# Optimization experiments

Hardware: AMD Instinct MI355X
Metric: run time of the kernel (lower is better)

The kernel has to match this reference:

```python
import jax, jax.numpy as jnp
import numpy as np


def setup_inputs() -> dict:
    key = jax.random.key(0)
    k_x, k_c = jax.random.split(key)
    ROWS, COLS = 4, 4
    B, N = 1024, 224
    x = jax.random.normal(k_x, (B, N, N), dtype=jnp.float32)
    # kaiming_normal_ on [rows, cols]: std = sqrt(2 / fan_in) with fan_in = cols
    coef = jax.random.normal(k_c, (ROWS, COLS), dtype=jnp.float32) * np.sqrt(2.0 / COLS)
    return {"x": x, "coef": coef}


def reference(x, coef):
    # x: [B, N, N]; coef: [rows, cols]
    rows, cols = coef.shape
    B, N, _ = x.shape

    # a_series[i] = matrix_power(x, i+2) for i in 0..rows-1 (the original also
    # computes power rows+2 but never uses it). Only the diagonals are needed:
    # diag(A ** p) == diag(A) ** p for elementwise power p.
    def step(P, _):
        Pn = jnp.matmul(P, x)                      # next matrix power, [B, N, N]
        return Pn, jnp.diagonal(Pn, axis1=-2, axis2=-1)  # [B, N]

    _, diags = jax.lax.scan(step, x, None, length=rows)  # [rows, B, N]
    d = jnp.transpose(diags, (1, 0, 2))                  # [B, rows, N]

    # traces[b, i, j] = sum_n diag(x^{i+2})[b, n] ** (j+1)
    exps = jnp.arange(1, cols + 1)                       # [cols]
    traces = jnp.sum(d[..., None] ** exps, axis=2)       # [B, rows, cols]

    # norm[i, j] = (N*N) ** (i + j + 2), computed in float (the original's int64
    # pow overflows for any realistic N; float is the intended math)
    i = jnp.arange(rows, dtype=x.dtype)[:, None]
    j = jnp.arange(cols, dtype=x.dtype)[None, :]
    norm = jnp.asarray(float(N * N), x.dtype) ** (i + j + 2.0)  # [rows, cols]

    return jnp.sum(coef * traces / norm, axis=(-1, -2))  # [B]
```

## Files before the change

kernel.cpp:

```cpp
#include <hip/hip_runtime.h>
#include <stdint.h>

#define B_ 1024
#define N_ 224
#define NN_ (N_ * N_)

typedef unsigned short u16;
typedef unsigned int u32;
typedef __attribute__((ext_vector_type(8))) short s8v;
typedef __attribute__((ext_vector_type(4))) float f4v;

__device__ __forceinline__ u16 f2bf(float f) {
  u32 u = __float_as_uint(f);
  u = (u + 0x7FFFu + ((u >> 16) & 1u)) >> 16;
  return (u16)u;
}
__device__ __forceinline__ float bf2f(u16 h) { return __uint_as_float((u32)h << 16); }
__device__ __forceinline__ float rec(u16 h, u16 l) { return bf2f(h) + bf2f(l); }

__device__ __forceinline__ void gload16(const void* g, void* l) {
  __builtin_amdgcn_global_load_lds(
      (const __attribute__((address_space(1))) uint32_t*)g,
      (__attribute__((address_space(3))) uint32_t*)l, 16, 0, 0);
}

__global__ __launch_bounds__(256) void splitT(const float* __restrict__ x,
                                              u16* __restrict__ xh, u16* __restrict__ xl,
                                              u16* __restrict__ xhT, u16* __restrict__ xlT) {
  __shared__ u16 th[32][34];
  __shared__ u16 tl[32][34];
  const int bid = blockIdx.x;
  const int mat = bid / 49, t2 = bid % 49;
  const int tm = (t2 / 7) * 32, tn = (t2 % 7) * 32;
  const int t = threadIdx.x;
  const int r = t >> 3, c4 = (t & 7) << 2;
  const size_t o = (size_t)mat * NN_ + (size_t)(tm + r) * N_ + tn + c4;
  const float4 v = *(const float4*)(x + o);
  u16 h0 = f2bf(v.x), h1 = f2bf(v.y), h2 = f2bf(v.z), h3 = f2bf(v.w);
  u16 l0 = f2bf(v.x - bf2f(h0)), l1 = f2bf(v.y - bf2f(h1));
  u16 l2 = f2bf(v.z - bf2f(h2)), l3 = f2bf(v.w - bf2f(h3));
  ushort4 hv = {h0, h1, h2, h3}, lv = {l0, l1, l2, l3};
  *(ushort4*)(xh + o) = hv;
  *(ushort4*)(xl + o) = lv;
  th[r][c4] = h0; th[r][c4 + 1] = h1; th[r][c4 + 2] = h2; th[r][c4 + 3] = h3;
  tl[r][c4] = l0; tl[r][c4 + 1] = l1; tl[r][c4 + 2] = l2; tl[r][c4 + 3] = l3;
  __syncthreads();
  ushort4 thv = {th[c4][r], th[c4 + 1][r], th[c4 + 2][r], th[c4 + 3][r]};
  ushort4 tlv = {tl[c4][r], tl[c4 + 1][r], tl[c4 + 2][r], tl[c4 + 3][r]};
  const size_t oT = (size_t)mat * NN_ + (size_t)(tn + r) * N_ + tm + c4;
  *(ushort4*)(xhT + oT) = thv;
  *(ushort4*)(xlT + oT) = tlv;
}

__global__ __launch_bounds__(256, 2) void gemmNT(const u16* __restrict__ Ah, const u16* __restrict__ Al,
                                                 const u16* __restrict__ BTh, const u16* __restrict__ BTl,
                                                 u16* __restrict__ Ch, u16* __restrict__ Cl) {
  __shared__ __align__(16) u16 As[2][128][64];
  __shared__ __align__(16) u16 Bs[2][128][64];

  const int nwg = gridDim.x, bid = blockIdx.x;
  const int q = nwg >> 3, rr = nwg & 7, xcd = bid & 7, pos = bid >> 3;
  const int wg = (xcd < rr) ? (xcd * (q + 1) + pos) : (rr * (q + 1) + (xcd - rr) * q + pos);
  const int mat = wg >> 2, t2 = wg & 3;
  const int m0 = (t2 & 1) * 96, n0 = (t2 >> 1) * 96;
  const size_t mo = (size_t)mat * NN_;
  const u16* A0 = Ah + mo;
  const u16* A1 = Al + mo;
  const u16* B0 = BTh + mo;
  const u16* B1 = BTl + mo;

  const int t = threadIdx.x;
  const int l = t & 63, w = t >> 6;
  const int wm = w & 1, wn = w >> 1;
  const int lg = l >> 4, l15 = l & 15;

  f4v acc[4][4];
#pragma unroll
  for (int i = 0; i < 4; ++i)
#pragma unroll
    for (int j = 0; j < 4; ++j) acc[i][j] = (f4v){0.f, 0.f, 0.f, 0.f};

  auto stage = [&](int buf, int k0) {
#pragma unroll
    for (int i = 0; i < 4; ++i) {
      const int s = i * 256 + t;
      const int row = s >> 3, p = s & 7;
      const int c = p ^ (row & 7);
      const int g = c & 3;
      const u16* ga = (c < 4) ? A0 : A1;
      const u16* gb = (c < 4) ? B0 : B1;
      gload16(ga + (size_t)(m0 + row) * N_ + k0 + g * 8, &As[buf][row][p * 8]);
      gload16(gb + (size_t)(n0 + row) * N_ + k0 + g * 8, &Bs[buf][row][p * 8]);
    }
  };

  stage(0, 0);
  int cur = 0;
  for (int kt = 0; kt < 7; ++kt) {
    __syncthreads();
    if (kt < 6) stage(cur ^ 1, (kt + 1) * 32);
    const u16(*Ab)[64] = As[cur];
    const u16(*Bb)[64] = Bs[cur];
    s8v ah[4], al[4], bh[4], bl[4];
#pragma unroll
    for (int i = 0; i < 4; ++i) {
      const int ra = wm * 64 + i * 16 + l15;
      const int rb = wn * 64 + i * 16 + l15;
      ah[i] = *(const s8v*)&Ab[ra][(lg ^ (ra & 7)) * 8];
      al[i] = *(const s8v*)&Ab[ra][((4 + lg) ^ (ra & 7)) * 8];
      bh[i] = *(const s8v*)&Bb[rb][(lg ^ (rb & 7)) * 8];
      bl[i] = *(const s8v*)&Bb[rb][((4 + lg) ^ (rb & 7)) * 8];
    }
#pragma unroll
    for (int i = 0; i < 4; ++i)
#pragma unroll
      for (int j = 0; j < 4; ++j) {
        acc[i][j] = __builtin_amdgcn_mfma_f32_16x16x32_bf16(ah[i], bh[j], acc[i][j], 0, 0, 0);
        acc[i][j] = __builtin_amdgcn_mfma_f32_16x16x32_bf16(ah[i], bl[j], acc[i][j], 0, 0, 0);
        acc[i][j] = __builtin_amdgcn_mfma_f32_16x16x32_bf16(al[i], bh[j], acc[i][j], 0, 0, 0);
      }
    cur ^= 1;
  }

  u16* cph = Ch + mo;
  u16* cpl = Cl + mo;
#pragma unroll
  for (int i = 0; i < 4; ++i)
#pragma unroll
    for (int j = 0; j < 4; ++j)
#pragma unroll
      for (int qd = 0; qd < 4; ++qd) {
        const float v = acc[i][j][qd];
        const int row = m0 + wm * 64 + i * 16 + lg * 4 + qd;
        const int col = n0 + wn * 64 + j * 16 + l15;
        const u16 hh = f2bf(v);
        const u16 ll = f2bf(v - bf2f(hh));
        cph[(size_t)row * N_ + col] = hh;
        cpl[(size_t)row * N_ + col] = ll;
      }
}

__global__ __launch_bounds__(256) void diagk(const u16* __restrict__ P2h, const u16* __restrict__ P2l,
                                             const u16* __restrict__ P3h, const u16* __restrict__ P3l,
                                             float* __restrict__ dg, int bBase) {
  __shared__ float s2[N_][17];
  __shared__ float s3[N_][17];
  const int b = blockIdx.x;
  const size_t mo = (size_t)b * NN_;
  const u16 *p2h = P2h + mo, *p2l = P2l + mo, *p3h = P3h + mo, *p3l = P3l + mo;
  const int gb = bBase + b;
  const int t = threadIdx.x;
  float d4 = 0.f, d5 = 0.f;
  for (int kb = 0; kb < N_; kb += 16) {
    __syncthreads();
#pragma unroll
    for (int base = 0; base < N_ * 16; base += 256) {
      const int f = base + t;
      const int n = f >> 4, j = f & 15;
      const size_t idx = (size_t)n * N_ + kb + j;
      s2[n][j] = rec(p2h[idx], p2l[idx]);
      s3[n][j] = rec(p3h[idx], p3l[idx]);
    }
    __syncthreads();
    if (t < N_) {
#pragma unroll
      for (int j = 0; j < 16; ++j) {
        const size_t ci = (size_t)(kb + j) * N_ + t;
        const float c2 = rec(p2h[ci], p2l[ci]);
        d4 = fmaf(s2[t][j], c2, d4);
        d5 = fmaf(s3[t][j], c2, d5);
      }
    }
  }
  if (t < N_) {
    const size_t di = (size_t)t * N_ + t;
    dg[((size_t)0 * B_ + gb) * N_ + t] = rec(p2h[di], p2l[di]);
    dg[((size_t)1 * B_ + gb) * N_ + t] = rec(p3h[di], p3l[di]);
    dg[((size_t)2 * B_ + gb) * N_ + t] = d4;
    dg[((size_t)3 * B_ + gb) * N_ + t] = d5;
  }
}

__global__ __launch_bounds__(256) void combine(const float* __restrict__ dg,
                                               const float* __restrict__ coef,
                                               float* __restrict__ out) {
  const int lane = threadIdx.x & 63;
  const int b = blockIdx.x * 4 + (threadIdx.x >> 6);
  float T[4][4] = {};
  for (int n = lane; n < N_; n += 64) {
#pragma unroll
    for (int i = 0; i < 4; ++i) {
      const float d = dg[((size_t)i * B_ + b) * N_ + n];
      float p = d;
#pragma unroll
      for (int j = 0; j < 4; ++j) {
        T[i][j] += p;
        p *= d;
      }
    }
  }
#pragma unroll
  for (int i = 0; i < 4; ++i)
#pragma unroll
    for (int j = 0; j < 4; ++j)
#pragma unroll
      for (int s = 32; s > 0; s >>= 1) T[i][j] += __shfl_xor(T[i][j], s, 64);
  if (lane == 0) {
    double acc = 0.0;
#pragma unroll
    for (int i = 0; i < 4; ++i)
#pragma unroll
      for (int j = 0; j < 4; ++j) {
        double norm = 1.0;
        for (int e = 0; e < i + j + 2; ++e) norm *= (double)(N_ * N_);
        acc += (double)coef[i * 4 + j] * ((double)T[i][j] / norm);
      }
    out[b] = (float)acc;
  }
}

extern "C" void kernel_launch(void* const* d_in, const int* in_sizes, int n_in,
                              void* d_out, int out_size, void* d_ws, size_t ws_size,
                              hipStream_t stream) {
  (void)in_sizes; (void)n_in; (void)out_size;
  const float* x = (const float*)d_in[0];
  const float* coef = (const float*)d_in[1];
  float* out = (float*)d_out;
  char* ws = (char*)d_ws;

  size_t off = 0;
  auto alloc = [&](size_t bytes) -> void* {
    off = (off + 255) & ~(size_t)255;
    void* p = ws + off;
    off += bytes;
    return p;
  };

  float* dg = (float*)alloc((size_t)4 * B_ * N_ * sizeof(float));

  const size_t perMat = (size_t)8 * NN_ * sizeof(u16);
  size_t avail = (ws_size > off + 256) ? (ws_size - off - 256) : 0;
  long long Cc = (long long)(avail / perMat);
  if (Cc < 1) Cc = 1;
  if (Cc > B_) Cc = B_;
  const int C = (int)Cc;
  const size_t matEls = (size_t)C * NN_;
  u16* xh = (u16*)alloc(matEls * 2);
  u16* xl = (u16*)alloc(matEls * 2);
  u16* xhT = (u16*)alloc(matEls * 2);
  u16* xlT = (u16*)alloc(matEls * 2);
  u16* P2h = (u16*)alloc(matEls * 2);
  u16* P2l = (u16*)alloc(matEls * 2);
  u16* P3h = (u16*)alloc(matEls * 2);
  u16* P3l = (u16*)alloc(matEls * 2);

  for (int b0 = 0; b0 < B_; b0 += C) {
    const int cb = (B_ - b0 < C) ? (B_ - b0) : C;
    splitT<<<49 * cb, 256, 0, stream>>>(x + (size_t)b0 * NN_, xh, xl, xhT, xlT);
    gemmNT<<<4 * cb, 256, 0, stream>>>(xh, xl, xhT, xlT, P2h, P2l);
    gemmNT<<<4 * cb, 256, 0, stream>>>(P2h, P2l, xhT, xlT, P3h, P3l);
    diagk<<<cb, 256, 0, stream>>>(P2h, P2l, P3h, P3l, dg, b0);
  }
  combine<<<256, 256, 0, stream>>>(dg, coef, out);
}
```

Measured before the change: 1.117 ms.

## Emit transposed P2 from GEMM epilogue and parallelize diagonal reduction across blocks

The first GEMM now also writes a transposed copy of P^2 (hi/lo bf16), so the diagonal kernel can compute row-dot-products of P2·P2 and P3·P2 with contiguous vectorized loads instead of LDS staging and strided column reads. The diag kernel is split into 7 blocks per matrix, with 8 lanes per row and a shuffle reduction, giving much more parallelism than one block per matrix. The cost is extra global writes from the GEMM epilogue (strided ushort4 stores) and a larger workspace per matrix, which may shrink the batch chunk size.

```diff
diff --git a/kernel.cpp b/kernel.cpp
--- a/kernel.cpp
+++ b/kernel.cpp
@@ -9,6 +9,7 @@
 typedef unsigned int u32;
 typedef __attribute__((ext_vector_type(8))) short s8v;
 typedef __attribute__((ext_vector_type(4))) float f4v;
+typedef __attribute__((ext_vector_type(8))) unsigned short us8;
 
 __device__ __forceinline__ u16 f2bf(float f) {
   u32 u = __float_as_uint(f);
@@ -54,7 +55,8 @@
 
 __global__ __launch_bounds__(256, 2) void gemmNT(const u16* __restrict__ Ah, const u16* __restrict__ Al,
                                                  const u16* __restrict__ BTh, const u16* __restrict__ BTl,
-                                                 u16* __restrict__ Ch, u16* __restrict__ Cl) {
+                                                 u16* __restrict__ Ch, u16* __restrict__ Cl,
+                                                 u16* __restrict__ CTh, u16* __restrict__ CTl) {
   __shared__ __align__(16) u16 As[2][128][64];
   __shared__ __align__(16) u16 Bs[2][128][64];
 
@@ -127,57 +129,73 @@
 #pragma unroll
   for (int i = 0; i < 4; ++i)
 #pragma unroll
-    for (int j = 0; j < 4; ++j)
+    for (int j = 0; j < 4; ++j) {
+      u16 hq[4], lq[4];
 #pragma unroll
       for (int qd = 0; qd < 4; ++qd) {
         const float v = acc[i][j][qd];
+        hq[qd] = f2bf(v);
+        lq[qd] = f2bf(v - bf2f(hq[qd]));
         const int row = m0 + wm * 64 + i * 16 + lg * 4 + qd;
         const int col = n0 + wn * 64 + j * 16 + l15;
-        const u16 hh = f2bf(v);
-        const u16 ll = f2bf(v - bf2f(hh));
-        cph[(size_t)row * N_ + col] = hh;
-        cpl[(size_t)row * N_ + col] = ll;
-      }
+        cph[(size_t)row * N_ + col] = hq[qd];
+        cpl[(size_t)row * N_ + col] = lq[qd];
+      }
+      if (CTh) {
+        const int row0 = m0 + wm * 64 + i * 16 + lg * 4;
+        const int col = n0 + wn * 64 + j * 16 + l15;
+        const ushort4 hv = {hq[0], hq[1], hq[2], hq[3]};
+        const ushort4 lv = {lq[0], lq[1], lq[2], lq[3]};
+        *(ushort4*)(CTh + mo + (size_t)col * N_ + row0) = hv;
+        *(ushort4*)(CTl + mo + (size_t)col * N_ + row0) = lv;
+      }
+    }
 }
 
 __global__ __launch_bounds__(256) void diagk(const u16* __restrict__ P2h, const u16* __restrict__ P2l,
+                                             const u16* __restrict__ P2Th, const u16* __restrict__ P2Tl,
                                              const u16* __restrict__ P3h, const u16* __restrict__ P3l,
                                              float* __restrict__ dg, int bBase) {
-  __shared__ float s2[N_][17];
-  __shared__ float s3[N_][17];
-  const int b = blockIdx.x;
+  const int bid = blockIdx.x;
+  const int b = bid / 7, p = bid % 7;
   const size_t mo = (size_t)b * NN_;
-  const u16 *p2h = P2h + mo, *p2l = P2l + mo, *p3h = P3h + mo, *p3l = P3l + mo;
   const int gb = bBase + b;
   const int t = threadIdx.x;
-  float d4 = 0.f, d5 = 0.f;
-  for (int kb = 0; kb < N_; kb += 16) {
-    __syncthreads();
-#pragma unroll
-    for (int base = 0; base < N_ * 16; base += 256) {
-      const int f = base + t;
-      const int n = f >> 4, j = f & 15;
-      const size_t idx = (size_t)n * N_ + kb + j;
-      s2[n][j] = rec(p2h[idx], p2l[idx]);
-      s3[n][j] = rec(p3h[idx], p3l[idx]);
-    }
-    __syncthreads();
-    if (t < N_) {
-#pragma unroll
-      for (int j = 0; j < 16; ++j) {
-        const size_t ci = (size_t)(kb + j) * N_ + t;
-        const float c2 = rec(p2h[ci], p2l[ci]);
-        d4 = fmaf(s2[t][j], c2, d4);
-        d5 = fmaf(s3[t][j], c2, d5);
-      }
-    }
-  }
-  if (t < N_) {
-    const size_t di = (size_t)t * N_ + t;
-    dg[((size_t)0 * B_ + gb) * N_ + t] = rec(p2h[di], p2l[di]);
-    dg[((size_t)1 * B_ + gb) * N_ + t] = rec(p3h[di], p3l[di]);
-    dg[((size_t)2 * B_ + gb) * N_ + t] = d4;
-    dg[((size_t)3 * B_ + gb) * N_ + t] = d5;
+  const int r8 = t >> 3, sub = t & 7;
+  const int n = p * 32 + r8;
+  const int gd = n >> 3;
+
+  float d4 = 0.f, d5 = 0.f, d2 = 0.f, d3 = 0.f;
+  bool own = false;
+  for (int g = sub; g < 28; g += 8) {
+    const size_t gi = mo + (size_t)n * N_ + g * 8;
+    const us8 a2h = *(const us8*)(P2h + gi), a2l = *(const us8*)(P2l + gi);
+    const us8 tth = *(const us8*)(P2Th + gi), ttl = *(const us8*)(P2Tl + gi);
+    const us8 a3h = *(const us8*)(P3h + gi), a3l = *(const us8*)(P3l + gi);
+#pragma unroll
+    for (int i = 0; i < 8; ++i) {
+      const float tv = rec(tth[i], ttl[i]);
+      d4 = fmaf(rec(a2h[i], a2l[i]), tv, d4);
+      d5 = fmaf(rec(a3h[i], a3l[i]), tv, d5);
+    }
+    if (g == gd) {
+      own = true;
+      d2 = rec(a2h[n & 7], a2l[n & 7]);
+      d3 = rec(a3h[n & 7], a3l[n & 7]);
+    }
+  }
+#pragma unroll
+  for (int m = 1; m < 8; m <<= 1) {
+    d4 += __shfl_xor(d4, m, 64);
+    d5 += __shfl_xor(d5, m, 64);
+  }
+  if (sub == 0) {
+    dg[((size_t)2 * B_ + gb) * N_ + n] = d4;
+    dg[((size_t)3 * B_ + gb) * N_ + n] = d5;
+  }
+  if (own) {
+    dg[((size_t)0 * B_ + gb) * N_ + n] = d2;
+    dg[((size_t)1 * B_ + gb) * N_ + n] = d3;
   }
 }
 
@@ -238,7 +256,7 @@
 
   float* dg = (float*)alloc((size_t)4 * B_ * N_ * sizeof(float));
 
-  const size_t perMat = (size_t)8 * NN_ * sizeof(u16);
+  const size_t perMat = (size_t)10 * NN_ * sizeof(u16);
   size_t avail = (ws_size > off + 256) ? (ws_size - off - 256) : 0;
   long long Cc = (long long)(avail / perMat);
   if (Cc < 1) Cc = 1;
@@ -251,15 +269,17 @@
   u16* xlT = (u16*)alloc(matEls * 2);
   u16* P2h = (u16*)alloc(matEls * 2);
   u16* P2l = (u16*)alloc(matEls * 2);
+  u16* P2Th = (u16*)alloc(matEls * 2);
+  u16* P2Tl = (u16*)alloc(matEls * 2);
   u16* P3h = (u16*)alloc(matEls * 2);
   u16* P3l = (u16*)alloc(matEls * 2);
 
   for (int b0 = 0; b0 < B_; b0 += C) {
     const int cb = (B_ - b0 < C) ? (B_ - b0) : C;
     splitT<<<49 * cb, 256, 0, stream>>>(x + (size_t)b0 * NN_, xh, xl, xhT, xlT);
-    gemmNT<<<4 * cb, 256, 0, stream>>>(xh, xl, xhT, xlT, P2h, P2l);
-    gemmNT<<<4 * cb, 256, 0, stream>>>(P2h, P2l, xhT, xlT, P3h, P3l);
-    diagk<<<cb, 256, 0, stream>>>(P2h, P2l, P3h, P3l, dg, b0);
+    gemmNT<<<4 * cb, 256, 0, stream>>>(xh, xl, xhT, xlT, P2h, P2l, P2Th, P2Tl);
+    gemmNT<<<4 * cb, 256, 0, stream>>>(P2h, P2l, xhT, xlT, P3h, P3l, nullptr, nullptr);
+    diagk<<<7 * cb, 256, 0, stream>>>(P2h, P2l, P2Th, P2Tl, P3h, P3l, dg, b0);
   }
   combine<<<256, 256, 0, stream>>>(dg, coef, out);
 }
```

New measurement: 1.010 ms. 1.11x faster.
